# Kernel tuning notes

Measured on AMD Instinct MI355X. Metric: run time of the kernel, lower is better.

The kernel has to match this reference:

```python
import jax, jax.numpy as jnp
import numpy as np

B, T, D = 512, 200, 512

def setup_inputs() -> dict:
    key = jax.random.key(0)
    k1, k2, k3 = jax.random.split(key, 3)
    inputs = jax.random.normal(k1, (B, T, D), dtype=jnp.float32)
    # Keras 'uniform' initializer -> U(-0.05, 0.05)
    W = jax.random.uniform(k2, (T, T), minval=-0.05, maxval=0.05, dtype=jnp.float32)
    b = jax.random.uniform(k3, (T,), minval=-0.05, maxval=0.05, dtype=jnp.float32)
    return {"inputs": inputs, "W": W, "b": b}

def reference(inputs, W, b):
    # x = permute(inputs, (0,2,1)) -> [B, D, T]; scores over timestep axis
    # a = softmax(tanh(x @ W + b)) along last axis (T)
    scores = jnp.tanh(jnp.einsum('btd,ts->bds', inputs, W) + b)  # [B, D, T]
    a = jax.nn.softmax(scores, axis=-1)                           # softmax over T
    # permute back to [B, T, D], elementwise multiply, sum over T -> [B, D]
    out = jnp.einsum('bdt,btd->bd', a, inputs)
    return out
```

## Files before the change

kernel.cpp:

```cpp
#include <hip/hip_runtime.h>
#include <cstdint>
#include <cstddef>

#define B_DIM 512
#define T_DIM 200
#define D_DIM 512
#define NPAD  208
#define NKG   28
#define NT    13
#define KS_STEPS 7
#define SLICE 3208

typedef short  short8  __attribute__((ext_vector_type(8)));
typedef float  floatx4 __attribute__((ext_vector_type(4)));

__device__ __forceinline__ unsigned short f2bf(float f) {
  unsigned int u = __float_as_uint(f);
  u += 0x7fffu + ((u >> 16) & 1u);
  return (unsigned short)(u >> 16);
}
__device__ __forceinline__ float bf2f(unsigned short h) {
  return __uint_as_float(((unsigned int)h) << 16);
}
__device__ __forceinline__ unsigned int cvt_pk_bf16(float a, float b) {
  unsigned int d;
  asm("v_cvt_pk_bf16_f32 %0, %1, %2" : "=v"(d) : "v"(a), "v"(b));
  return d;
}

__global__ void prep_w_kernel(const float* __restrict__ W,
                              unsigned short* __restrict__ wf) {
  int idx = blockIdx.x * blockDim.x + threadIdx.x;
  if (idx >= NKG * 8 * NPAD) return;
  int k = idx / NPAD;
  int n = idx - k * NPAD;
  float v = (k < T_DIM && n < T_DIM) ? W[k * T_DIM + n] : 0.0f;
  wf[((size_t)(k >> 3) * NPAD + n) * 8 + (k & 7)] = f2bf(v);
}

__global__ __launch_bounds__(256, 4)
void attn_kernel(const float* __restrict__ X,
                 const unsigned short* __restrict__ wf,
                 const float* __restrict__ bias,
                 float* __restrict__ out) {
  __shared__ __align__(16) unsigned short Xs[4 * SLICE];
  __shared__ __align__(16) float comb[4][4][64][2];

  const int tid  = threadIdx.x;
  const int wv   = tid >> 6;
  const int lane = tid & 63;
  const int l15  = lane & 15;
  const int g    = lane >> 4;

  const int bid  = blockIdx.x;
  const int bb   = bid >> 3;
  const int dblk = (bid & 7) << 6;

  {
    const float* xb = X + (size_t)bb * (T_DIM * D_DIM) + dblk;
    const int c4 = tid & 15;
    const int t0 = tid >> 4;
    const float* src = xb + (size_t)t0 * D_DIM + (c4 << 2);
    unsigned short* dst = Xs + (c4 >> 2) * SLICE
                        + ((t0 >> 3) * 16 + ((c4 & 3) << 2)) * 8 + (t0 & 7);
    #pragma unroll
    for (int it = 0; it < 13; ++it) {
      if (it < 12 || tid < 128) {
        float4 v = *(const float4*)src;
        unsigned int w01 = cvt_pk_bf16(v.x, v.y);
        unsigned int w23 = cvt_pk_bf16(v.z, v.w);
        dst[0]  = (unsigned short)(w01 & 0xffffu);
        dst[8]  = (unsigned short)(w01 >> 16);
        dst[16] = (unsigned short)(w23 & 0xffffu);
        dst[24] = (unsigned short)(w23 >> 16);
      }
      src += 16 * D_DIM;
      dst += 256;
    }
  }
  __syncthreads();

  const int nt0 = 3 * wv;
  const int ntw = 3 + (wv == 3);

  floatx4 acc[4][4];
  #pragma unroll
  for (int h = 0; h < 4; ++h)
    #pragma unroll
    for (int j = 0; j < 4; ++j)
      acc[h][j] = (floatx4){0.f, 0.f, 0.f, 0.f};

  const unsigned short* wk = wf + ((size_t)g * NPAD + nt0 * 16 + l15) * 8;

  #pragma unroll
  for (int ks = 0; ks < KS_STEPS; ++ks) {
    const int kg = ks * 4 + g;
    short8 b[4];
    #pragma unroll
    for (int j = 0; j < 4; ++j)
      if (j < ntw) b[j] = *(const short8*)(wk + (size_t)ks * (4 * NPAD * 8) + j * 128);
    const bool av = (ks < 6) || (g == 0);
    short8 a[4];
    #pragma unroll
    for (int h = 0; h < 4; ++h)
      a[h] = av ? *(const short8*)&Xs[h * SLICE + (kg * 16 + l15) * 8]
                : (short8){0, 0, 0, 0, 0, 0, 0, 0};
    #pragma unroll
    for (int j = 0; j < 4; ++j)
      if (j < ntw) {
        #pragma unroll
        for (int h = 0; h < 4; ++h)
          acc[h][j] = __builtin_amdgcn_mfma_f32_16x16x32_bf16(a[h], b[j], acc[h][j], 0, 0, 0);
      }
  }

  float part[4][4], rs[4][4];
  #pragma unroll
  for (int h = 0; h < 4; ++h)
    #pragma unroll
    for (int r = 0; r < 4; ++r) { part[h][r] = 0.f; rs[h][r] = 0.f; }

  #pragma unroll
  for (int j = 0; j < 4; ++j) {
    if (j < ntw) {
      const int nt = nt0 + j;
      const int t  = nt * 16 + l15;
      const bool valid = (t < T_DIM);
      const int tc = valid ? t : (T_DIM - 1);
      const float bb2 = 2.0f * bias[tc];
      const unsigned short* xp = &Xs[((tc >> 3) * 16) * 8 + (tc & 7)];
      #pragma unroll
      for (int r = 0; r < 4; ++r) {
        const int m = g * 4 + r;
        #pragma unroll
        for (int h = 0; h < 4; ++h) {
          float u  = __expf(__builtin_fmaf(acc[h][j][r], 2.0f, bb2));
          float v  = __fdividef(2.0f, u + 1.0f);
          float p0 = __expf(-v);
          float p  = valid ? p0 : 0.0f;
          rs[h][r]   += p;
          part[h][r] += p * bf2f(xp[h * SLICE + m * 8]);
        }
      }
    }
  }
  #pragma unroll
  for (int off = 1; off <= 2; off <<= 1)
    #pragma unroll
    for (int h = 0; h < 4; ++h)
      #pragma unroll
      for (int r = 0; r < 4; ++r) {
        part[h][r] += __shfl_xor(part[h][r], off, 16);
        rs[h][r]   += __shfl_xor(rs[h][r],   off, 16);
      }

  if ((l15 & 3) == 0) {
    const int q = l15 >> 2;
    #pragma unroll
    for (int h = 0; h < 4; ++h)
      #pragma unroll
      for (int r = 0; r < 4; ++r) {
        const int idx = h * 16 + g * 4 + r;
        comb[wv][q][idx][0] = part[h][r];
        comb[wv][q][idx][1] = rs[h][r];
      }
  }
  __syncthreads();

  if (tid < 64) {
    float ps = 0.f, ss = 0.f;
    #pragma unroll
    for (int w = 0; w < 4; ++w)
      #pragma unroll
      for (int q = 0; q < 4; ++q) {
        const float2 v = *(const float2*)&comb[w][q][tid][0];
        ps += v.x;
        ss += v.y;
      }
    out[(size_t)bb * D_DIM + dblk + tid] = ps * __frcp_rn(ss);
  }
}

extern "C" void kernel_launch(void* const* d_in, const int* in_sizes, int n_in,
                              void* d_out, int out_size, void* d_ws, size_t ws_size,
                              hipStream_t stream) {
  const float* X  = (const float*)d_in[0];
  const float* W  = (const float*)d_in[1];
  const float* bs = (const float*)d_in[2];
  float* out = (float*)d_out;
  unsigned short* wf = (unsigned short*)d_ws;

  const int wtot = NKG * 8 * NPAD;
  hipLaunchKernelGGL(prep_w_kernel, dim3((wtot + 255) / 256), dim3(256), 0, stream,
                     W, wf);
  hipLaunchKernelGGL(attn_kernel, dim3(4096), dim3(256), 0, stream,
                     X, wf, bs, out);
}
```

Before: 315.3 us.

## Make attention kernel persistent per batch with double-buffered X tiles and 8 waves

Each block now handles one whole batch row, looping over eight 64-column D chunks instead of one chunk per block. It uses 512 threads, with the T tiles split across 8 waves, and double-buffers the bf16 X slice in LDS. Global loads for the next chunk are issued into registers before the tanh/softmax epilogue so their latency overlaps compute. The trade-off is fewer blocks (512), meaning less parallelism per CU, plus higher register pressure and an extra barrier per chunk.

```diff
diff --git a/kernel.cpp b/kernel.cpp
--- a/kernel.cpp
+++ b/kernel.cpp
@@ -14,13 +14,13 @@
 typedef short  short8  __attribute__((ext_vector_type(8)));
 typedef float  floatx4 __attribute__((ext_vector_type(4)));
 
+__device__ __forceinline__ float bf2f(unsigned short h) {
+  return __uint_as_float(((unsigned int)h) << 16);
+}
 __device__ __forceinline__ unsigned short f2bf(float f) {
   unsigned int u = __float_as_uint(f);
   u += 0x7fffu + ((u >> 16) & 1u);
   return (unsigned short)(u >> 16);
-}
-__device__ __forceinline__ float bf2f(unsigned short h) {
-  return __uint_as_float(((unsigned int)h) << 16);
 }
 __device__ __forceinline__ unsigned int cvt_pk_bf16(float a, float b) {
   unsigned int d;
@@ -38,13 +38,13 @@
   wf[((size_t)(k >> 3) * NPAD + n) * 8 + (k & 7)] = f2bf(v);
 }
 
-__global__ __launch_bounds__(256, 4)
+__global__ __launch_bounds__(512, 4)
 void attn_kernel(const float* __restrict__ X,
                  const unsigned short* __restrict__ wf,
                  const float* __restrict__ bias,
                  float* __restrict__ out) {
-  __shared__ __align__(16) unsigned short Xs[4 * SLICE];
-  __shared__ __align__(16) float comb[4][4][64][2];
+  __shared__ __align__(16) unsigned short Xa[2][4 * SLICE];
+  __shared__ __align__(16) float comb[8][2][64][2];
 
   const int tid  = threadIdx.x;
   const int wv   = tid >> 6;
@@ -52,132 +52,169 @@
   const int l15  = lane & 15;
   const int g    = lane >> 4;
 
-  const int bid  = blockIdx.x;
-  const int bb   = bid >> 3;
-  const int dblk = (bid & 7) << 6;
-
+  const int bb = blockIdx.x;
+
+  const int c4 = tid & 15;
+  const int t0 = tid >> 4;
+  const float* src0 = X + (size_t)bb * (T_DIM * D_DIM)
+                      + (size_t)t0 * D_DIM + (c4 << 2);
+  const int dbase = (c4 >> 2) * SLICE
+                  + ((t0 >> 3) * 16 + ((c4 & 3) << 2)) * 8 + (t0 & 7);
+
+  const int nt0 = (wv < 5) ? 2 * wv : (wv + 5);
+  const int ntw = (wv < 5) ? 2 : 1;
+
+  float bb2[2];
+  int   xb16[2];
+  bool  val[2];
+  #pragma unroll
+  for (int j = 0; j < 2; ++j) {
+    const int t = (nt0 + j) * 16 + l15;
+    val[j] = (j < ntw) && (t < T_DIM);
+    const int tc = (t < T_DIM) ? t : (T_DIM - 1);
+    bb2[j]  = 2.0f * bias[tc];
+    xb16[j] = ((tc >> 3) * 16) * 8 + (tc & 7);
+  }
+
+  const unsigned short* wk = wf + ((size_t)g * NPAD + nt0 * 16 + l15) * 8;
+
+  float4 pf[7];
+  #pragma unroll
+  for (int it = 0; it < 7; ++it)
+    if (it < 6 || tid < 128) pf[it] = *(const float4*)(src0 + (size_t)it * 32 * D_DIM);
   {
-    const float* xb = X + (size_t)bb * (T_DIM * D_DIM) + dblk;
-    const int c4 = tid & 15;
-    const int t0 = tid >> 4;
-    const float* src = xb + (size_t)t0 * D_DIM + (c4 << 2);
-    unsigned short* dst = Xs + (c4 >> 2) * SLICE
-                        + ((t0 >> 3) * 16 + ((c4 & 3) << 2)) * 8 + (t0 & 7);
-    #pragma unroll
-    for (int it = 0; it < 13; ++it) {
-      if (it < 12 || tid < 128) {
-        float4 v = *(const float4*)src;
-        unsigned int w01 = cvt_pk_bf16(v.x, v.y);
-        unsigned int w23 = cvt_pk_bf16(v.z, v.w);
+    unsigned short* dst = &Xa[0][dbase];
+    #pragma unroll
+    for (int it = 0; it < 7; ++it) {
+      if (it < 6 || tid < 128) {
+        unsigned int w01 = cvt_pk_bf16(pf[it].x, pf[it].y);
+        unsigned int w23 = cvt_pk_bf16(pf[it].z, pf[it].w);
         dst[0]  = (unsigned short)(w01 & 0xffffu);
         dst[8]  = (unsigned short)(w01 >> 16);
         dst[16] = (unsigned short)(w23 & 0xffffu);
         dst[24] = (unsigned short)(w23 >> 16);
       }
-      src += 16 * D_DIM;
-      dst += 256;
+      dst += 512;
     }
   }
   __syncthreads();
 
-  const int nt0 = 3 * wv;
-  const int ntw = 3 + (wv == 3);
-
-  floatx4 acc[4][4];
-  #pragma unroll
-  for (int h = 0; h < 4; ++h)
-    #pragma unroll
-    for (int j = 0; j < 4; ++j)
-      acc[h][j] = (floatx4){0.f, 0.f, 0.f, 0.f};
-
-  const unsigned short* wk = wf + ((size_t)g * NPAD + nt0 * 16 + l15) * 8;
-
-  #pragma unroll
-  for (int ks = 0; ks < KS_STEPS; ++ks) {
-    const int kg = ks * 4 + g;
-    short8 b[4];
-    #pragma unroll
-    for (int j = 0; j < 4; ++j)
-      if (j < ntw) b[j] = *(const short8*)(wk + (size_t)ks * (4 * NPAD * 8) + j * 128);
-    const bool av = (ks < 6) || (g == 0);
-    short8 a[4];
+  #pragma unroll 2
+  for (int n = 0; n < 8; ++n) {
+    const int cur = n & 1;
+    const unsigned short* Xw = &Xa[cur][0];
+
+    floatx4 acc[4][2];
     #pragma unroll
     for (int h = 0; h < 4; ++h)
-      a[h] = av ? *(const short8*)&Xs[h * SLICE + (kg * 16 + l15) * 8]
-                : (short8){0, 0, 0, 0, 0, 0, 0, 0};
-    #pragma unroll
-    for (int j = 0; j < 4; ++j)
+      #pragma unroll
+      for (int j = 0; j < 2; ++j)
+        acc[h][j] = (floatx4){0.f, 0.f, 0.f, 0.f};
+
+    #pragma unroll
+    for (int ks = 0; ks < KS_STEPS; ++ks) {
+      const int kg = ks * 4 + g;
+      short8 b0 = *(const short8*)(wk + (size_t)ks * (4 * NPAD * 8));
+      short8 b1;
+      if (ntw == 2) b1 = *(const short8*)(wk + (size_t)ks * (4 * NPAD * 8) + 128);
+      const bool av = (ks < 6) || (g == 0);
+      short8 a[4];
+      #pragma unroll
+      for (int h = 0; h < 4; ++h)
+        a[h] = av ? *(const short8*)&Xw[h * SLICE + (kg * 16 + l15) * 8]
+                  : (short8){0, 0, 0, 0, 0, 0, 0, 0};
+      #pragma unroll
+      for (int h = 0; h < 4; ++h)
+        acc[h][0] = __builtin_amdgcn_mfma_f32_16x16x32_bf16(a[h], b0, acc[h][0], 0, 0, 0);
+      if (ntw == 2) {
+        #pragma unroll
+        for (int h = 0; h < 4; ++h)
+          acc[h][1] = __builtin_amdgcn_mfma_f32_16x16x32_bf16(a[h], b1, acc[h][1], 0, 0, 0);
+      }
+    }
+
+    if (n < 7) {
+      const float* src = src0 + ((n + 1) << 6);
+      #pragma unroll
+      for (int it = 0; it < 7; ++it)
+        if (it < 6 || tid < 128) pf[it] = *(const float4*)(src + (size_t)it * 32 * D_DIM);
+    }
+
+    float part[4][4], rs[4][4];
+    #pragma unroll
+    for (int h = 0; h < 4; ++h)
+      #pragma unroll
+      for (int r = 0; r < 4; ++r) { part[h][r] = 0.f; rs[h][r] = 0.f; }
+
+    #pragma unroll
+    for (int j = 0; j < 2; ++j) {
       if (j < ntw) {
-        #pragma unroll
-        for (int h = 0; h < 4; ++h)
-          acc[h][j] = __builtin_amdgcn_mfma_f32_16x16x32_bf16(a[h], b[j], acc[h][j], 0, 0, 0);
-      }
-  }
-
-  float part[4][4], rs[4][4];
-  #pragma unroll
-  for (int h = 0; h < 4; ++h)
-    #pragma unroll
-    for (int r = 0; r < 4; ++r) { part[h][r] = 0.f; rs[h][r] = 0.f; }
-
-  #pragma unroll
-  for (int j = 0; j < 4; ++j) {
-    if (j < ntw) {
-      const int nt = nt0 + j;
-      const int t  = nt * 16 + l15;
-      const bool valid = (t < T_DIM);
-      const int tc = valid ? t : (T_DIM - 1);
-      const float bb2 = 2.0f * bias[tc];
-      const unsigned short* xp = &Xs[((tc >> 3) * 16) * 8 + (tc & 7)];
-      #pragma unroll
-      for (int r = 0; r < 4; ++r) {
-        const int m = g * 4 + r;
-        #pragma unroll
-        for (int h = 0; h < 4; ++h) {
-          float u  = __expf(__builtin_fmaf(acc[h][j][r], 2.0f, bb2));
-          float v  = __fdividef(2.0f, u + 1.0f);
-          float p0 = __expf(-v);
-          float p  = valid ? p0 : 0.0f;
-          rs[h][r]   += p;
-          part[h][r] += p * bf2f(xp[h * SLICE + m * 8]);
-        }
-      }
-    }
-  }
-  #pragma unroll
-  for (int off = 1; off <= 2; off <<= 1)
-    #pragma unroll
-    for (int h = 0; h < 4; ++h)
-      #pragma unroll
-      for (int r = 0; r < 4; ++r) {
-        part[h][r] += __shfl_xor(part[h][r], off, 16);
-        rs[h][r]   += __shfl_xor(rs[h][r],   off, 16);
-      }
-
-  if ((l15 & 3) == 0) {
-    const int q = l15 >> 2;
-    #pragma unroll
-    for (int h = 0; h < 4; ++h)
-      #pragma unroll
-      for (int r = 0; r < 4; ++r) {
-        const int idx = h * 16 + g * 4 + r;
-        comb[wv][q][idx][0] = part[h][r];
-        comb[wv][q][idx][1] = rs[h][r];
-      }
-  }
-  __syncthreads();
-
-  if (tid < 64) {
-    float ps = 0.f, ss = 0.f;
-    #pragma unroll
-    for (int w = 0; w < 4; ++w)
-      #pragma unroll
-      for (int q = 0; q < 4; ++q) {
-        const float2 v = *(const float2*)&comb[w][q][tid][0];
-        ps += v.x;
-        ss += v.y;
-      }
-    out[(size_t)bb * D_DIM + dblk + tid] = ps * __frcp_rn(ss);
+        const unsigned short* xp = &Xw[xb16[j]];
+        #pragma unroll
+        for (int r = 0; r < 4; ++r) {
+          const int m = g * 4 + r;
+          #pragma unroll
+          for (int h = 0; h < 4; ++h) {
+            float u  = __expf(__builtin_fmaf(acc[h][j][r], 2.0f, bb2[j]));
+            float v  = __fdividef(2.0f, u + 1.0f);
+            float p  = val[j] ? __expf(-v) : 0.0f;
+            rs[h][r]   += p;
+            part[h][r] += p * bf2f(xp[h * SLICE + m * 8]);
+          }
+        }
+      }
+    }
+    #pragma unroll
+    for (int off = 1; off <= 4; off <<= 1)
+      #pragma unroll
+      for (int h = 0; h < 4; ++h)
+        #pragma unroll
+        for (int r = 0; r < 4; ++r) {
+          part[h][r] += __shfl_xor(part[h][r], off, 16);
+          rs[h][r]   += __shfl_xor(rs[h][r],   off, 16);
+        }
+    if ((l15 & 7) == 0) {
+      const int q = l15 >> 3;
+      #pragma unroll
+      for (int h = 0; h < 4; ++h)
+        #pragma unroll
+        for (int r = 0; r < 4; ++r) {
+          const int idx = h * 16 + g * 4 + r;
+          comb[wv][q][idx][0] = part[h][r];
+          comb[wv][q][idx][1] = rs[h][r];
+        }
+    }
+    __syncthreads();
+
+    if (tid < 64) {
+      float ps = 0.f, ss = 0.f;
+      #pragma unroll
+      for (int w = 0; w < 8; ++w)
+        #pragma unroll
+        for (int q = 0; q < 2; ++q) {
+          const float2 v = *(const float2*)&comb[w][q][tid][0];
+          ps += v.x;
+          ss += v.y;
+        }
+      out[(size_t)bb * D_DIM + (n << 6) + tid] = ps * __frcp_rn(ss);
+    }
+
+    if (n < 7) {
+      unsigned short* dst = &Xa[cur ^ 1][dbase];
+      #pragma unroll
+      for (int it = 0; it < 7; ++it) {
+        if (it < 6 || tid < 128) {
+          unsigned int w01 = cvt_pk_bf16(pf[it].x, pf[it].y);
+          unsigned int w23 = cvt_pk_bf16(pf[it].z, pf[it].w);
+          dst[0]  = (unsigned short)(w01 & 0xffffu);
+          dst[8]  = (unsigned short)(w01 >> 16);
+          dst[16] = (unsigned short)(w23 & 0xffffu);
+          dst[24] = (unsigned short)(w23 >> 16);
+        }
+        dst += 512;
+      }
+      __syncthreads();
+    }
   }
 }
 
@@ -193,6 +230,6 @@
   const int wtot = NKG * 8 * NPAD;
   hipLaunchKernelGGL(prep_w_kernel, dim3((wtot + 255) / 256), dim3(256), 0, stream,
                      W, wf);
-  hipLaunchKernelGGL(attn_kernel, dim3(4096), dim3(256), 0, stream,
+  hipLaunchKernelGGL(attn_kernel, dim3(512), dim3(512), 0, stream,
                      X, wf, bs, out);
 }
```

Measured after the change: 350.6 us. 11.2% more time.
